# Kernel optimization log

Hardware: AMD Instinct MI355X
Metric: run time of the kernel (lower is better)

## Reference

```python
import jax, jax.numpy as jnp
import numpy as np

B, S, H, NH, HD = 64, 200, 1024, 16, 64
MAX_LEN = 200
FF = 4 * H


def _ln(x, g, b):
    m = x.mean(-1, keepdims=True)
    v = ((x - m) ** 2).mean(-1, keepdims=True)
    return (x - m) / jnp.sqrt(v + 1e-5) * g + b


def setup_inputs() -> dict:
    key = jax.random.key(0)
    k = jax.random.split(key, 24)
    s = 0.02
    f32 = jnp.float32
    return {
        "x": jax.random.normal(k[0], (B, S, H), f32),
        "time": jax.random.uniform(k[1], (B, S, 1), dtype=f32),
        "wq": jax.random.normal(k[2], (H, H), f32) * s,
        "bq": jnp.zeros((H,), f32),
        "wk": jax.random.normal(k[3], (H, H), f32) * s,
        "bk": jnp.zeros((H,), f32),
        "wv": jax.random.normal(k[4], (H, H), f32) * s,
        "bv": jnp.zeros((H,), f32),
        "wo": jax.random.normal(k[5], (H, H), f32) * s,
        "bo": jnp.zeros((H,), f32),
        "wt": jax.random.normal(k[6], (1, H), f32) * s,
        "bt": jnp.zeros((H,), f32),
        "pos_embed": jax.random.normal(k[7], (2 * MAX_LEN - 1, HD), f32) * s,
        "g1": jnp.ones((H,), f32),
        "be1": jnp.zeros((H,), f32),
        "g2": jnp.ones((H,), f32),
        "be2": jnp.zeros((H,), f32),
        "w1": jax.random.normal(k[8], (H, FF), f32) * s,
        "bf1": jnp.zeros((FF,), f32),
        "w2": jax.random.normal(k[9], (FF, H), f32) * s,
        "bf2": jnp.zeros((H,), f32),
    }


def reference(x, time, wq, bq, wk, bk, wv, bv, wo, bo, wt, bt, pos_embed,
              g1, be1, g2, be2, w1, bf1, w2, bf2):
    b, s, hs = x.shape
    residual = x
    h = _ln(x, g1, be1)
    h = h + time @ wt + bt  # time embedding added post-LN
    q = (h @ wq + bq).reshape(b, s, NH, HD).transpose(0, 2, 1, 3)  # [b,h,s,d]
    k = (h @ wk + bk).reshape(b, s, NH, HD).transpose(0, 2, 1, 3)
    v = (h @ wv + bv).reshape(b, s, NH, HD).transpose(0, 2, 1, 3)
    scale = np.float32(1.0 / np.sqrt(HD))
    scores = jnp.einsum('bhqd,bhkd->bhqk', q, k) * scale
    # gathered relative position bias (NOT scaled, added after scaling)
    idx = jnp.arange(s)
    rel = jnp.clip(idx[:, None] - idx[None, :] + (MAX_LEN - 1), 0, 2 * MAX_LEN - 2)
    rel_emb = pos_embed[rel]  # [s, s, HD]
    scores = scores + jnp.einsum('bhqd,qkd->bhqk', q, rel_emb)
    causal_mask = jnp.triu(jnp.ones((s, s), bool), 1)
    scores = jnp.where(causal_mask, jnp.float32(-1e9), scores)
    attn = jax.nn.softmax(scores, axis=-1)
    ctx = jnp.einsum('bhqk,bhkd->bhqd', attn, v)
    ctx = ctx.transpose(0, 2, 1, 3).reshape(b, s, hs)
    out = ctx @ wo + bo + residual
    res2 = out
    h2 = _ln(out, g2, be2)
    ff = jax.nn.gelu(h2 @ w1 + bf1, approximate=False) @ w2 + bf2
    return ff + res2
```

## Files before the change

kernel.cpp:

```cpp
#include <hip/hip_runtime.h>

#define B_SZ   64
#define S_LEN  200
#define H_DIM  1024
#define NHEAD  16
#define HDIM   64
#define FF_DIM 4096
#define NROWS  (B_SZ * S_LEN)

typedef __bf16 bf16x8 __attribute__((ext_vector_type(8)));
typedef float  f32x4  __attribute__((ext_vector_type(4)));

#define GLOBAL_AS __attribute__((address_space(1)))
#define LDS_AS    __attribute__((address_space(3)))

__device__ __forceinline__ void g2lds16(const void* g, void* l) {
  __builtin_amdgcn_global_load_lds((const GLOBAL_AS void*)g, (LDS_AS void*)l, 16, 0, 0);
}

__device__ __forceinline__ float b2f(ushort u) {
  return __uint_as_float(((unsigned int)u) << 16);
}
__device__ __forceinline__ ushort f2b(float f) {
  unsigned int u = __float_as_uint(f);
  u += 0x7fffu + ((u >> 16) & 1u);
  return (ushort)(u >> 16);
}
__device__ __forceinline__ bf16x8 ld_g16(const ushort* p) {
  union { uint4 u; bf16x8 v; } r; r.u = *(const uint4*)p; return r.v;
}
__device__ __forceinline__ bf16x8 ld_lds8x2(const ushort* p) {
  union { uint2 u[2]; bf16x8 v; } r;
  r.u[0] = *(const uint2*)p;
  r.u[1] = *(const uint2*)(p + 4);
  return r.v;
}

__global__ __launch_bounds__(256) void transpose_to_bf16(
    const float* __restrict__ w, ushort* __restrict__ wt, int K, int N) {
  __shared__ float tile[32][33];
  int nb = blockIdx.x * 32, kb = blockIdx.y * 32;
  int tx = threadIdx.x, ty = threadIdx.y;
#pragma unroll
  for (int i = 0; i < 4; ++i) {
    int k = kb + ty + i * 8;
    tile[ty + i * 8][tx] = w[(size_t)k * N + nb + tx];
  }
  __syncthreads();
#pragma unroll
  for (int i = 0; i < 4; ++i) {
    int n = nb + ty + i * 8;
    wt[(size_t)n * K + kb + tx] = f2b(tile[tx][ty + i * 8]);
  }
}

__global__ void concat_bias(const float* __restrict__ bq, const float* __restrict__ bk,
                            const float* __restrict__ bv, float* __restrict__ o) {
  int i = blockIdx.x * 256 + threadIdx.x;
  if (i < 1024) o[i] = bq[i];
  else if (i < 2048) o[i] = bk[i - 1024];
  else if (i < 3072) o[i] = bv[i - 2048];
}

__global__ void pos_to_bf16(const float* __restrict__ pos, ushort* __restrict__ pb) {
  int i = blockIdx.x * 256 + threadIdx.x;
  pb[i] = f2b(pos[(size_t)199 * 64 + i]);
}

template <int HAS_TIME>
__global__ __launch_bounds__(256) void ln_kernel(
    const float* __restrict__ x, const float* __restrict__ g, const float* __restrict__ be,
    const float* __restrict__ tv, const float* __restrict__ wt, const float* __restrict__ bt,
    ushort* __restrict__ out) {
  int r = blockIdx.x, t = threadIdx.x;
  const float4* xr = (const float4*)(x + (size_t)r * H_DIM);
  float4 xv = xr[t];
  float s  = xv.x + xv.y + xv.z + xv.w;
  float s2 = xv.x * xv.x + xv.y * xv.y + xv.z * xv.z + xv.w * xv.w;
#pragma unroll
  for (int off = 32; off; off >>= 1) {
    s  += __shfl_xor(s, off);
    s2 += __shfl_xor(s2, off);
  }
  __shared__ float red[8];
  int lane = t & 63, wid = t >> 6;
  if (lane == 0) { red[wid] = s; red[4 + wid] = s2; }
  __syncthreads();
  float S  = red[0] + red[1] + red[2] + red[3];
  float S2 = red[4] + red[5] + red[6] + red[7];
  float m    = S * (1.0f / H_DIM);
  float var  = S2 * (1.0f / H_DIM) - m * m;
  float rstd = rsqrtf(var + 1e-5f);
  float tval = HAS_TIME ? tv[r] : 0.0f;
  float4 gv = ((const float4*)g)[t];
  float4 bv = ((const float4*)be)[t];
  float v0 = (xv.x - m) * rstd * gv.x + bv.x;
  float v1 = (xv.y - m) * rstd * gv.y + bv.y;
  float v2 = (xv.z - m) * rstd * gv.z + bv.z;
  float v3 = (xv.w - m) * rstd * gv.w + bv.w;
  if (HAS_TIME) {
    float4 wv = ((const float4*)wt)[t];
    float4 btv = ((const float4*)bt)[t];
    v0 += tval * wv.x + btv.x;
    v1 += tval * wv.y + btv.y;
    v2 += tval * wv.z + btv.z;
    v3 += tval * wv.w + btv.w;
  }
  ushort4 o;
  o.x = f2b(v0); o.y = f2b(v1); o.z = f2b(v2); o.w = f2b(v3);
  ((ushort4*)(out + (size_t)r * H_DIM))[t] = o;
}

template <int EPI>
__global__ __launch_bounds__(256) void gemm_bt(
    const ushort* __restrict__ A, const ushort* __restrict__ Bt,
    const float* __restrict__ bias, void* __restrict__ Cv,
    const float* __restrict__ resid, int M, int N, int K) {
  __shared__ __align__(16) ushort As[2 * 128 * 32];
  __shared__ __align__(16) ushort Bs[2 * 128 * 32];
  int t = threadIdx.x;
  int lane = t & 63, wave = t >> 6;
  int wm = wave >> 1, wn = wave & 1;
  int r15 = lane & 15, quad = lane >> 4;
  size_t row0 = (size_t)blockIdx.y * 128;
  size_t col0 = (size_t)blockIdx.x * 128;

  int srow = (lane >> 2), scol = (lane & 3) * 8;
  const ushort* ga0 = A  + (row0 + wave * 32 +      srow) * K + scol;
  const ushort* ga1 = A  + (row0 + wave * 32 + 16 + srow) * K + scol;
  const ushort* gb0 = Bt + (col0 + wave * 32 +      srow) * K + scol;
  const ushort* gb1 = Bt + (col0 + wave * 32 + 16 + srow) * K + scol;
  ushort* la0 = As + (wave * 32) * 32;
  ushort* la1 = As + (wave * 32 + 16) * 32;
  ushort* lb0 = Bs + (wave * 32) * 32;
  ushort* lb1 = Bs + (wave * 32 + 16) * 32;

  f32x4 acc[4][4] = {};

  for (int k0 = 0; k0 < K; k0 += 64) {
#pragma unroll
    for (int kh = 0; kh < 2; ++kh) {
      int go = k0 + kh * 32, lo = kh * 4096;
      g2lds16(ga0 + go, la0 + lo);
      g2lds16(ga1 + go, la1 + lo);
      g2lds16(gb0 + go, lb0 + lo);
      g2lds16(gb1 + go, lb1 + lo);
    }
    __syncthreads();
#pragma unroll
    for (int kh = 0; kh < 2; ++kh) {
      bf16x8 af[4], bfr[4];
#pragma unroll
      for (int i = 0; i < 4; ++i)
        af[i] = *(const bf16x8*)&As[kh * 4096 + (wm * 64 + i * 16 + r15) * 32 + quad * 8];
#pragma unroll
      for (int j = 0; j < 4; ++j)
        bfr[j] = *(const bf16x8*)&Bs[kh * 4096 + (wn * 64 + j * 16 + r15) * 32 + quad * 8];
#pragma unroll
      for (int i = 0; i < 4; ++i)
#pragma unroll
        for (int j = 0; j < 4; ++j)
          acc[i][j] = __builtin_amdgcn_mfma_f32_16x16x32_bf16(af[i], bfr[j], acc[i][j], 0, 0, 0);
    }
    __syncthreads();
  }

  int mbase = (int)row0 + wm * 64;
  int nbase = (int)col0 + wn * 64;
#pragma unroll
  for (int i = 0; i < 4; ++i) {
#pragma unroll
    for (int j = 0; j < 4; ++j) {
      int col = nbase + j * 16 + r15;
      float bb = bias[col];
#pragma unroll
      for (int ii = 0; ii < 4; ++ii) {
        int row = mbase + i * 16 + quad * 4 + ii;
        size_t idx = (size_t)row * N + col;
        float v = acc[i][j][ii] + bb;
        if constexpr (EPI == 0) {
          ((ushort*)Cv)[idx] = f2b(v);
        } else if constexpr (EPI == 1) {
          float gl = 0.5f * v * (1.0f + erff(v * 0.70710678118f));
          ((ushort*)Cv)[idx] = f2b(gl);
        } else {
          ((float*)Cv)[idx] = v + resid[idx];
        }
      }
    }
  }
}

#define PW_STRIDE 228
__global__ __launch_bounds__(256) void attn_kernel(
    const ushort* __restrict__ qkv, const ushort* __restrict__ pos_bf,
    ushort* __restrict__ ctx) {
  int bh = blockIdx.x;
  int b = bh >> 4, h = bh & 15;
  __shared__ ushort Vt[64][PW_STRIDE];
  __shared__ ushort Pw[4][16][PW_STRIDE];
  int t = threadIdx.x, lane = t & 63, wave = t >> 6;
  int r15 = lane & 15, quad = lane >> 4;
  const size_t base = ((size_t)b * S_LEN) * 3072 + (size_t)h * 64;

  for (int i = t; i < 64 * 28; i += 256) Vt[i / 28][200 + (i % 28)] = 0;
  for (int i = t; i < 800; i += 256) {
    int kp = i >> 3, d0 = (i & 7) * 8;
    int k = kp * 2;
    union { uint4 v; ushort u[8]; } r0, r1;
    r0.v = *(const uint4*)&qkv[base + (size_t)k * 3072 + 2048 + d0];
    r1.v = *(const uint4*)&qkv[base + (size_t)(k + 1) * 3072 + 2048 + d0];
#pragma unroll
    for (int j = 0; j < 8; ++j) {
      ushort2 w2; w2.x = r0.u[j]; w2.y = r1.u[j];
      *(ushort2*)&Vt[d0 + j][k] = w2;
    }
  }
  __syncthreads();

  for (int qt = wave; qt < 13; qt += 4) {
    int q0 = qt * 16;
    int qrow = q0 + r15; if (qrow > 199) qrow = 199;
    const ushort* qp = qkv + base + (size_t)qrow * 3072;
    bf16x8 aq0 = ld_g16(qp + quad * 8);
    bf16x8 aq1 = ld_g16(qp + 32 + quad * 8);
    ushort* pw = &Pw[wave][0][0];

#pragma unroll
    for (int dt = 0; dt < 13; ++dt) {
      if (dt > qt) continue;
      int prow = dt * 16 + r15; if (prow > 199) prow = 199;
      const ushort* pp = pos_bf + (size_t)prow * 64;
      bf16x8 p0 = ld_g16(pp + quad * 8);
      bf16x8 p1 = ld_g16(pp + 32 + quad * 8);
      f32x4 tt = {};
      tt = __builtin_amdgcn_mfma_f32_16x16x32_bf16(aq0, p0, tt, 0, 0, 0);
      tt = __builtin_amdgcn_mfma_f32_16x16x32_bf16(aq1, p1, tt, 0, 0, 0);
#pragma unroll
      for (int ii = 0; ii < 4; ++ii)
        pw[(quad * 4 + ii) * PW_STRIDE + dt * 16 + r15] = f2b(tt[ii]);
    }

    f32x4 sreg[13];
    float rowmax[4] = {-3.0e38f, -3.0e38f, -3.0e38f, -3.0e38f};
#pragma unroll
    for (int kt = 0; kt < 13; ++kt) {
      if (kt > qt) continue;
      int krow = kt * 16 + r15; if (krow > 199) krow = 199;
      const ushort* kp = qkv + base + (size_t)krow * 3072 + 1024;
      bf16x8 k0 = ld_g16(kp + quad * 8);
      bf16x8 k1 = ld_g16(kp + 32 + quad * 8);
      f32x4 s = {};
      s = __builtin_amdgcn_mfma_f32_16x16x32_bf16(aq0, k0, s, 0, 0, 0);
      s = __builtin_amdgcn_mfma_f32_16x16x32_bf16(aq1, k1, s, 0, 0, 0);
      int k = kt * 16 + r15;
#pragma unroll
      for (int ii = 0; ii < 4; ++ii) {
        int q = q0 + quad * 4 + ii;
        float v;
        if (k <= q) {
          v = s[ii] * 0.125f + b2f(pw[(quad * 4 + ii) * PW_STRIDE + (q - k)]);
        } else {
          v = -1.0e30f;
        }
        s[ii] = v;
        rowmax[ii] = fmaxf(rowmax[ii], v);
      }
      sreg[kt] = s;
    }
#pragma unroll
    for (int off = 8; off; off >>= 1)
#pragma unroll
      for (int ii = 0; ii < 4; ++ii)
        rowmax[ii] = fmaxf(rowmax[ii], __shfl_xor(rowmax[ii], off));

    float rsum[4] = {0.f, 0.f, 0.f, 0.f};
#pragma unroll
    for (int kt = 0; kt < 13; ++kt) {
      if (kt > qt) continue;
#pragma unroll
      for (int ii = 0; ii < 4; ++ii) {
        float e = __expf(sreg[kt][ii] - rowmax[ii]);
        rsum[ii] += e;
        pw[(quad * 4 + ii) * PW_STRIDE + kt * 16 + r15] = f2b(e);
      }
    }
    if ((qt & 1) == 0) {
#pragma unroll
      for (int ii = 0; ii < 4; ++ii)
        pw[(quad * 4 + ii) * PW_STRIDE + (qt + 1) * 16 + r15] = 0;
    }
#pragma unroll
    for (int off = 8; off; off >>= 1)
#pragma unroll
      for (int ii = 0; ii < 4; ++ii)
        rsum[ii] += __shfl_xor(rsum[ii], off);
    float rinv[4];
#pragma unroll
    for (int ii = 0; ii < 4; ++ii) rinv[ii] = 1.0f / rsum[ii];

    int nk = (q0 + 15) / 32 + 1;
    f32x4 acc[4] = {};
#pragma unroll
    for (int k32 = 0; k32 < 7; ++k32) {
      if (k32 >= nk) continue;
      bf16x8 ap = ld_lds8x2(&pw[r15 * PW_STRIDE + k32 * 32 + quad * 8]);
#pragma unroll
      for (int n = 0; n < 4; ++n) {
        bf16x8 bv = ld_lds8x2(&Vt[n * 16 + r15][k32 * 32 + quad * 8]);
        acc[n] = __builtin_amdgcn_mfma_f32_16x16x32_bf16(ap, bv, acc[n], 0, 0, 0);
      }
    }
#pragma unroll
    for (int n = 0; n < 4; ++n)
#pragma unroll
      for (int ii = 0; ii < 4; ++ii) {
        int q = q0 + quad * 4 + ii;
        if (q < S_LEN)
          ctx[((size_t)(b * S_LEN + q)) * H_DIM + h * 64 + n * 16 + r15] =
              f2b(acc[n][ii] * rinv[ii]);
      }
  }
}

extern "C" void kernel_launch(void* const* d_in, const int* in_sizes, int n_in,
                              void* d_out, int out_size, void* d_ws, size_t ws_size,
                              hipStream_t stream) {
  (void)in_sizes; (void)n_in; (void)out_size; (void)ws_size;
  const float* x    = (const float*)d_in[0];
  const float* timev= (const float*)d_in[1];
  const float* wq   = (const float*)d_in[2];
  const float* bq   = (const float*)d_in[3];
  const float* wk   = (const float*)d_in[4];
  const float* bk   = (const float*)d_in[5];
  const float* wv   = (const float*)d_in[6];
  const float* bv   = (const float*)d_in[7];
  const float* wo   = (const float*)d_in[8];
  const float* bo   = (const float*)d_in[9];
  const float* wt   = (const float*)d_in[10];
  const float* bt   = (const float*)d_in[11];
  const float* pos  = (const float*)d_in[12];
  const float* g1   = (const float*)d_in[13];
  const float* be1  = (const float*)d_in[14];
  const float* g2   = (const float*)d_in[15];
  const float* be2  = (const float*)d_in[16];
  const float* w1   = (const float*)d_in[17];
  const float* bf1  = (const float*)d_in[18];
  const float* w2   = (const float*)d_in[19];
  const float* bf2  = (const float*)d_in[20];

  char* ws = (char*)d_ws;
  ushort* wqkv_t = (ushort*)ws;   ws += (size_t)3072 * 1024 * 2;
  ushort* wo_t   = (ushort*)ws;   ws += (size_t)1024 * 1024 * 2;
  ushort* w1_t   = (ushort*)ws;   ws += (size_t)4096 * 1024 * 2;
  ushort* w2_t   = (ushort*)ws;   ws += (size_t)1024 * 4096 * 2;
  float*  bqkv   = (float*)ws;    ws += (size_t)16384;
  ushort* pos_bf = (ushort*)ws;   ws += (size_t)200 * 64 * 2;
  char* r1 = ws;                  ws += (size_t)NROWS * 3072 * 2;
  ushort* qkv  = (ushort*)r1;
  ushort* h2   = (ushort*)r1;
  ushort* gbuf = (ushort*)(r1 + (size_t)NROWS * H_DIM * 2);
  char* r2 = ws;                  ws += (size_t)NROWS * 1024 * 2;
  ushort* hbf = (ushort*)r2;
  ushort* ctx = (ushort*)r2;
  float* res2 = (float*)d_out;

  dim3 tb(32, 8);
  transpose_to_bf16<<<dim3(32, 32), tb, 0, stream>>>(wq, wqkv_t,                 1024, 1024);
  transpose_to_bf16<<<dim3(32, 32), tb, 0, stream>>>(wk, wqkv_t + 1024 * 1024,   1024, 1024);
  transpose_to_bf16<<<dim3(32, 32), tb, 0, stream>>>(wv, wqkv_t + 2048 * 1024,   1024, 1024);
  transpose_to_bf16<<<dim3(32, 32), tb, 0, stream>>>(wo, wo_t,                   1024, 1024);
  transpose_to_bf16<<<dim3(128, 32), tb, 0, stream>>>(w1, w1_t,                  1024, 4096);
  transpose_to_bf16<<<dim3(32, 128), tb, 0, stream>>>(w2, w2_t,                  4096, 1024);
  concat_bias<<<12, 256, 0, stream>>>(bq, bk, bv, bqkv);
  pos_to_bf16<<<50, 256, 0, stream>>>(pos, pos_bf);

  ln_kernel<1><<<NROWS, 256, 0, stream>>>(x, g1, be1, timev, wt, bt, hbf);

  gemm_bt<0><<<dim3(24, 100), 256, 0, stream>>>(hbf, wqkv_t, bqkv, qkv, nullptr,
                                                NROWS, 3072, 1024);
  attn_kernel<<<B_SZ * NHEAD, 256, 0, stream>>>(qkv, pos_bf, ctx);

  gemm_bt<2><<<dim3(8, 100), 256, 0, stream>>>(ctx, wo_t, bo, res2, x,
                                               NROWS, 1024, 1024);
  ln_kernel<0><<<NROWS, 256, 0, stream>>>(res2, g2, be2, nullptr, nullptr, nullptr, h2);

  for (int c = 0; c < 2; ++c) {
    size_t ro = (size_t)c * 6400;
    gemm_bt<1><<<dim3(32, 50), 256, 0, stream>>>(h2 + ro * 1024, w1_t, bf1, gbuf, nullptr,
                                                 6400, 4096, 1024);
    gemm_bt<2><<<dim3(8, 50), 256, 0, stream>>>(gbuf, w2_t, bf2, (float*)d_out + ro * 1024,
                                                res2 + ro * 1024, 6400, 1024, 4096);
  }
}
```

Baseline: 798.2 us.

## Add 256x256-tile 8-wave GEMM with ping-pong LDS pipeline for QKV, out-proj, FF1

Adds a new GEMM kernel with 256x256 output tiles across 512 threads. It double-buffers LDS through direct global-to-LDS loads and interleaves fragment reads, prefetch issue and MFMA blocks with barriers and s_setprio. The QKV, output-projection and FF1 GEMMs now use it, while FF2 keeps the old kernel. Larger tiles raise operand reuse and cut global traffic per FLOP, at the cost of fewer blocks: 600, 200 and 400 in the three grids. That risks underfilling the GPU's compute units, especially for the out-projection.

```diff
diff --git a/kernel.cpp b/kernel.cpp
--- a/kernel.cpp
+++ b/kernel.cpp
@@ -189,6 +189,162 @@
       }
     }
   }
+}
+
+template <int IB>
+__device__ __forceinline__ void mfma_blk(f32x4 (&acc)[8][4],
+                                         const bf16x8 (&af)[4], const bf16x8 (&bfr)[4]) {
+#pragma unroll
+  for (int i = 0; i < 4; ++i)
+#pragma unroll
+    for (int j = 0; j < 4; ++j)
+      acc[IB + i][j] =
+          __builtin_amdgcn_mfma_f32_16x16x32_bf16(af[i], bfr[j], acc[IB + i][j], 0, 0, 0);
+}
+
+__device__ __forceinline__ bf16x8 rdfrag(const ushort* plane, int r, int quad) {
+  return *(const bf16x8*)(plane + r * 32 + ((quad ^ ((r >> 1) & 3)) << 3));
+}
+
+#define WAITVM4() asm volatile("s_waitcnt vmcnt(4)" ::: "memory")
+#define WAITVM0() asm volatile("s_waitcnt vmcnt(0)" ::: "memory")
+
+template <int EPI>
+__global__ __launch_bounds__(512) void gemm256(
+    const ushort* __restrict__ A, const ushort* __restrict__ Bt,
+    const float* __restrict__ bias, void* __restrict__ Cv,
+    const float* __restrict__ resid, int M, int N, int K) {
+  __shared__ __align__(16) ushort lds[2][2][2][2][4096];
+  const int t = threadIdx.x;
+  const int lane = t & 63, wave = t >> 6;
+  const int wm = wave >> 2;
+  const int wn = wave & 3;
+  const int bh = wn >> 1;
+  const int r15 = lane & 15, quad = lane >> 4;
+  const size_t row0 = (size_t)blockIdx.y * 256;
+  const size_t col0 = (size_t)blockIdx.x * 256;
+
+  const int gwA = wave & 3;
+  const int gwB = ((wave >> 1) & 2) | (wave & 1);
+
+  const ushort *gA0, *gA1, *gB0, *gB1;
+  {
+    int p0 = gwA * 128 + lane;
+    int p1 = p0 + 64;
+    int ra0 = p0 >> 2, sa0 = (p0 & 3) ^ ((p0 >> 3) & 3);
+    int ra1 = p1 >> 2, sa1 = (p1 & 3) ^ ((p1 >> 3) & 3);
+    gA0 = A + (row0 + wm * 128 + ra0) * K + sa0 * 8;
+    gA1 = A + (row0 + wm * 128 + ra1) * K + sa1 * 8;
+    int q0 = gwB * 128 + lane;
+    int q1 = q0 + 64;
+    int rb0 = q0 >> 2, sb0 = (q0 & 3) ^ ((q0 >> 3) & 3);
+    int rb1 = q1 >> 2, sb1 = (q1 & 3) ^ ((q1 >> 3) & 3);
+    gB0 = Bt + (col0 + bh * 128 + rb0) * K + sb0 * 8;
+    gB1 = Bt + (col0 + bh * 128 + rb1) * K + sb1 * 8;
+  }
+  const int ldsA0 = gwA * 1024, ldsA1 = gwA * 1024 + 512;
+  const int ldsB0 = gwB * 1024, ldsB1 = gwB * 1024 + 512;
+
+#define STAGE_A(nb_, skh_, kof_)                                        \
+  do {                                                                  \
+    g2lds16(gA0 + (kof_) + (skh_) * 32, &lds[nb_][0][wm][skh_][ldsA0]); \
+    g2lds16(gA1 + (kof_) + (skh_) * 32, &lds[nb_][0][wm][skh_][ldsA1]); \
+  } while (0)
+#define STAGE_B(nb_, skh_, kof_)                                        \
+  do {                                                                  \
+    g2lds16(gB0 + (kof_) + (skh_) * 32, &lds[nb_][1][bh][skh_][ldsB0]); \
+    g2lds16(gB1 + (kof_) + (skh_) * 32, &lds[nb_][1][bh][skh_][ldsB1]); \
+  } while (0)
+
+  f32x4 acc[8][4] = {};
+  const int NT = K >> 6;
+
+  STAGE_A(0, 0, 0);
+  STAGE_B(0, 0, 0);
+  STAGE_A(0, 1, 0);
+  STAGE_B(0, 1, 0);
+  WAITVM4();
+  __builtin_amdgcn_s_barrier();
+
+  for (int tt = 0; tt < NT; ++tt) {
+    const int cb = tt & 1, nb = cb ^ 1;
+    const int kn = (tt + 1) << 6;
+    const bool pf = (tt + 1 < NT);
+    const ushort* pA0 = &lds[cb][0][wm][0][0];
+    const ushort* pB0 = &lds[cb][1][bh][0][0];
+    const ushort* pA1 = &lds[cb][0][wm][1][0];
+    const ushort* pB1 = &lds[cb][1][bh][1][0];
+    bf16x8 af[4], bfr[4];
+
+#pragma unroll
+    for (int j = 0; j < 4; ++j) bfr[j] = rdfrag(pB0, (wn & 1) * 64 + j * 16 + r15, quad);
+#pragma unroll
+    for (int i = 0; i < 4; ++i) af[i] = rdfrag(pA0, i * 16 + r15, quad);
+    if (pf) STAGE_A(nb, 0, kn);
+    __builtin_amdgcn_s_barrier();
+    __builtin_amdgcn_s_setprio(1);
+    mfma_blk<0>(acc, af, bfr);
+    __builtin_amdgcn_s_setprio(0);
+    __builtin_amdgcn_s_barrier();
+
+#pragma unroll
+    for (int i = 0; i < 4; ++i) af[i] = rdfrag(pA0, 64 + i * 16 + r15, quad);
+    if (pf) STAGE_B(nb, 0, kn);
+    __builtin_amdgcn_s_barrier();
+    __builtin_amdgcn_s_setprio(1);
+    mfma_blk<4>(acc, af, bfr);
+    __builtin_amdgcn_s_setprio(0);
+    if (tt == NT - 1) { WAITVM0(); } else { WAITVM4(); }
+    __builtin_amdgcn_s_barrier();
+
+#pragma unroll
+    for (int j = 0; j < 4; ++j) bfr[j] = rdfrag(pB1, (wn & 1) * 64 + j * 16 + r15, quad);
+#pragma unroll
+    for (int i = 0; i < 4; ++i) af[i] = rdfrag(pA1, i * 16 + r15, quad);
+    if (pf) STAGE_A(nb, 1, kn);
+    __builtin_amdgcn_s_barrier();
+    __builtin_amdgcn_s_setprio(1);
+    mfma_blk<0>(acc, af, bfr);
+    __builtin_amdgcn_s_setprio(0);
+    __builtin_amdgcn_s_barrier();
+
+#pragma unroll
+    for (int i = 0; i < 4; ++i) af[i] = rdfrag(pA1, 64 + i * 16 + r15, quad);
+    if (pf) STAGE_B(nb, 1, kn);
+    __builtin_amdgcn_s_barrier();
+    __builtin_amdgcn_s_setprio(1);
+    mfma_blk<4>(acc, af, bfr);
+    __builtin_amdgcn_s_setprio(0);
+    if (pf) WAITVM4();
+    __builtin_amdgcn_s_barrier();
+  }
+
+  int mbase = (int)row0 + wm * 128;
+  int nbase = (int)col0 + wn * 64;
+#pragma unroll
+  for (int j = 0; j < 4; ++j) {
+    int col = nbase + j * 16 + r15;
+    float bb = bias[col];
+#pragma unroll
+    for (int i = 0; i < 8; ++i) {
+#pragma unroll
+      for (int ii = 0; ii < 4; ++ii) {
+        int row = mbase + i * 16 + quad * 4 + ii;
+        size_t idx = (size_t)row * N + col;
+        float v = acc[i][j][ii] + bb;
+        if constexpr (EPI == 0) {
+          ((ushort*)Cv)[idx] = f2b(v);
+        } else if constexpr (EPI == 1) {
+          float gl = 0.5f * v * (1.0f + erff(v * 0.70710678118f));
+          ((ushort*)Cv)[idx] = f2b(gl);
+        } else {
+          ((float*)Cv)[idx] = v + resid[idx];
+        }
+      }
+    }
+  }
+#undef STAGE_A
+#undef STAGE_B
 }
 
 #define PW_STRIDE 228
@@ -377,17 +533,17 @@
 
   ln_kernel<1><<<NROWS, 256, 0, stream>>>(x, g1, be1, timev, wt, bt, hbf);
 
-  gemm_bt<0><<<dim3(24, 100), 256, 0, stream>>>(hbf, wqkv_t, bqkv, qkv, nullptr,
-                                                NROWS, 3072, 1024);
+  gemm256<0><<<dim3(12, 50), 512, 0, stream>>>(hbf, wqkv_t, bqkv, qkv, nullptr,
+                                               NROWS, 3072, 1024);
   attn_kernel<<<B_SZ * NHEAD, 256, 0, stream>>>(qkv, pos_bf, ctx);
 
-  gemm_bt<2><<<dim3(8, 100), 256, 0, stream>>>(ctx, wo_t, bo, res2, x,
-                                               NROWS, 1024, 1024);
+  gemm256<2><<<dim3(4, 50), 512, 0, stream>>>(ctx, wo_t, bo, res2, x,
+                                              NROWS, 1024, 1024);
   ln_kernel<0><<<NROWS, 256, 0, stream>>>(res2, g2, be2, nullptr, nullptr, nullptr, h2);
 
   for (int c = 0; c < 2; ++c) {
     size_t ro = (size_t)c * 6400;
-    gemm_bt<1><<<dim3(32, 50), 256, 0, stream>>>(h2 + ro * 1024, w1_t, bf1, gbuf, nullptr,
+    gemm256<1><<<dim3(16, 25), 512, 0, stream>>>(h2 + ro * 1024, w1_t, bf1, gbuf, nullptr,
                                                  6400, 4096, 1024);
     gemm_bt<2><<<dim3(8, 50), 256, 0, stream>>>(gbuf, w2_t, bf2, (float*)d_out + ro * 1024,
                                                 res2 + ro * 1024, 6400, 1024, 4096);
```

Measured after the change: 813.8 us. No clear change (+2.0%).
